# Kernel tuning notes

Hardware: AMD Instinct MI355X
Metric: run time of the kernel (lower is better)

Reference implementation:

```python
import jax, jax.numpy as jnp
import numpy as np

B, T, H, V, GEN = 1024, 64, 512, 1024, 100


def setup_inputs() -> dict:
    key = jax.random.key(0)
    ks = jax.random.split(key, 16)
    u = lambda k, shape, fan: jax.random.uniform(k, shape, jnp.float32, -1.0 / np.sqrt(fan), 1.0 / np.sqrt(fan))
    inp = {}
    inp["input"] = jax.random.normal(ks[0], (B, 1), jnp.float32)
    tok = jax.random.randint(ks[1], (B, T), 0, V)
    inp["onehots"] = jax.nn.one_hot(tok, V, dtype=jnp.float32)
    inp["digits"] = jax.random.randint(ks[2], (B,), 0, 10)
    inp["teacher"] = 0
    # expander_h / expander_c : Linear(1, H)
    inp["Wh"] = u(ks[3], (H, 1), 1); inp["bh"] = u(ks[4], (H,), 1)
    inp["Wc"] = u(ks[5], (H, 1), 1); inp["bc"] = u(ks[6], (H,), 1)
    # LSTM(V -> H), torch init: U(-1/sqrt(H), 1/sqrt(H)), gate order i,f,g,o
    inp["W_ih"] = u(ks[7], (4 * H, V), H); inp["W_hh"] = u(ks[8], (4 * H, H), H)
    inp["b_ih"] = u(ks[9], (4 * H,), H); inp["b_hh"] = u(ks[10], (4 * H,), H)
    # hidden2word: Linear(H, GEN) -> ReLU -> Linear(GEN, V) -> LogSoftmax
    inp["W1"] = u(ks[11], (GEN, H), H); inp["b1"] = u(ks[12], (GEN,), H)
    inp["W2"] = u(ks[13], (V, GEN), GEN); inp["b2"] = u(ks[14], (V,), GEN)
    return inp


def reference(input, onehots, digits, teacher, Wh, bh, Wc, bc, W_ih, W_hh, b_ih, b_hh, W1, b1, W2, b2):
    h0 = input @ Wh.T + bh  # [B,H]
    c0 = input @ Wc.T + bc  # [B,H]
    b = b_ih + b_hh

    def cell(h, c, x):
        g = x @ W_ih.T + h @ W_hh.T + b  # [B,4H]
        i, f, gg, o = jnp.split(g, 4, axis=-1)
        c = jax.nn.sigmoid(f) * c + jax.nn.sigmoid(i) * jnp.tanh(gg)
        h = jax.nn.sigmoid(o) * jnp.tanh(c)
        return h, c

    def head(h):  # hidden2word, log-softmax over vocab
        return jax.nn.log_softmax(jax.nn.relu(h @ W1.T + b1) @ W2.T + b2, axis=-1)

    if teacher:
        def step(carry, x):
            h, c = carry
            h, c = cell(h, c, x)
            return (h, c), head(h)
        _, logps = jax.lax.scan(step, (h0, c0), jnp.swapaxes(onehots, 0, 1))
    else:
        def step(carry, _):
            h, c, x = carry
            h, c = cell(h, c, x)
            logp = head(h)  # [B,V]
            nxt = jax.nn.one_hot(jnp.argmax(logp, axis=-1), V, dtype=logp.dtype)
            return (h, c, nxt), logp
        _, logps = jax.lax.scan(step, (h0, c0, onehots[:, 0, :]), None, length=T)
    return logps  # [T, B, V] == stacked vocab_list
```

## Files before the change

### kernel.cpp

```cpp
#include <hip/hip_runtime.h>
#include <math.h>

#define B_   1024
#define T_   64
#define H_   512
#define V_   1024
#define GEN_ 100
#define FH   2048
#define KC   1536

static constexpr size_t MB = 1024ull * 1024;
static constexpr size_t OFF_G    = 0;
static constexpr size_t OFF_C    = 16 * MB;
static constexpr size_t OFF_WIHT = 18 * MB;
static constexpr size_t OFF_ACAT = 26 * MB;
static constexpr size_t OFF_BCAT = 29 * MB;
static constexpr size_t OFF_BSUM = 35 * MB;
static constexpr size_t OFF_TOK  = 35 * MB + 8192;
static constexpr size_t OFF_H    = 36 * MB;

typedef __attribute__((ext_vector_type(8))) short short8v;
typedef __attribute__((ext_vector_type(4))) float f32x4;

__device__ __forceinline__ float sigf(float x) { return 1.0f / (1.0f + expf(-x)); }

__device__ __forceinline__ unsigned short f2bf(float f) {
    unsigned int u = __float_as_uint(f);
    return (unsigned short)((u + 0x7FFFu + ((u >> 16) & 1u)) >> 16);
}
__device__ __forceinline__ float bf2f(unsigned short b) {
    return __uint_as_float(((unsigned int)b) << 16);
}

__device__ __forceinline__ void gload16(const void* g, void* l) {
    __builtin_amdgcn_global_load_lds((const __attribute__((address_space(1))) void*)g,
                                     (__attribute__((address_space(3))) void*)l, 16, 0, 0);
}

__global__ __launch_bounds__(256) void k_init(const float* __restrict__ input,
                                              const float* __restrict__ Wh, const float* __restrict__ bh,
                                              const float* __restrict__ Wc, const float* __restrict__ bc,
                                              const float* __restrict__ bih, const float* __restrict__ bhh,
                                              float* __restrict__ cbuf, short* __restrict__ acat,
                                              float* __restrict__ bsum) {
    int idx = blockIdx.x * 256 + threadIdx.x;
    int b = idx >> 9, j = idx & (H_ - 1);
    float x = input[b];
    float h0 = x * Wh[j] + bh[j];
    cbuf[idx] = x * Wc[j] + bc[j];
    unsigned short hi = f2bf(h0);
    unsigned short lo = f2bf(h0 - bf2f(hi));
    short* ar = acat + (size_t)b * KC;
    ar[j] = (short)hi; ar[512 + j] = (short)hi; ar[1024 + j] = (short)lo;
    if (idx < FH) bsum[idx] = bih[idx] + bhh[idx];
}

__global__ __launch_bounds__(256) void k_tok0(const float* __restrict__ onehots, int* __restrict__ tok) {
    int idx = blockIdx.x * 256 + threadIdx.x;
    int b = idx >> 10, v = idx & (V_ - 1);
    if (onehots[(size_t)b * (T_ * V_) + v] > 0.5f) tok[b] = v;
}

__global__ __launch_bounds__(256) void k_transpose(const float* __restrict__ Wih, float* __restrict__ WihT) {
    int idx = blockIdx.x * 256 + threadIdx.x;
    int v = idx >> 11, n = idx & (FH - 1);
    WihT[idx] = Wih[(size_t)n * V_ + v];
}

__global__ __launch_bounds__(256) void k_prep(const float* __restrict__ Whh, short* __restrict__ bcat) {
    int idx = blockIdx.x * 256 + threadIdx.x;
    int n = idx >> 9, k = idx & (H_ - 1);
    float w = Whh[idx];
    unsigned short hi = f2bf(w);
    unsigned short lo = f2bf(w - bf2f(hi));
    short* br = bcat + (size_t)n * KC;
    br[k] = (short)hi; br[512 + k] = (short)lo; br[1024 + k] = (short)hi;
}

__global__ __launch_bounds__(256) void k_cell(const float* __restrict__ gbuf,
                                              float* __restrict__ cbuf, short* __restrict__ acat,
                                              const float* __restrict__ WihT, const float* __restrict__ bsum,
                                              const int* __restrict__ tok,
                                              float* __restrict__ hbuf) {
    const int tid = threadIdx.x;
    const int b = blockIdx.x * 2 + (tid >> 7);
    const int j = (tid & 127) << 2;
    const int tk = tok[b];
    const float* __restrict__ wr = WihT + (size_t)tk * FH;
    const size_t base = (size_t)b * FH;

    float4 g4[4];
#pragma unroll
    for (int gi_ = 0; gi_ < 4; ++gi_) {
        const int off = gi_ * 512 + j;
        float4 a0 = *(const float4*)&gbuf[base + off];
        float4 wv = *(const float4*)&wr[off];
        float4 bs = *(const float4*)&bsum[off];
        g4[gi_].x = a0.x + wv.x + bs.x;
        g4[gi_].y = a0.y + wv.y + bs.y;
        g4[gi_].z = a0.z + wv.z + bs.z;
        g4[gi_].w = a0.w + wv.w + bs.w;
    }
    float4 co = *(const float4*)&cbuf[(size_t)b * H_ + j];
    float cn[4], hn[4];
    const float* gi_p = (const float*)&g4[0];
    const float* gf_p = (const float*)&g4[1];
    const float* gg_p = (const float*)&g4[2];
    const float* go_p = (const float*)&g4[3];
    const float* co_p = (const float*)&co;
#pragma unroll
    for (int e = 0; e < 4; ++e) {
        cn[e] = sigf(gf_p[e]) * co_p[e] + sigf(gi_p[e]) * tanhf(gg_p[e]);
        hn[e] = sigf(go_p[e]) * tanhf(cn[e]);
    }
    *(float4*)&cbuf[(size_t)b * H_ + j] = make_float4(cn[0], cn[1], cn[2], cn[3]);
    *(float4*)&hbuf[(size_t)b * H_ + j] = make_float4(hn[0], hn[1], hn[2], hn[3]);
    unsigned long long hh = 0ull, ll = 0ull;
#pragma unroll
    for (int e = 0; e < 4; ++e) {
        unsigned short hi = f2bf(hn[e]);
        unsigned short lo = f2bf(hn[e] - bf2f(hi));
        hh |= (unsigned long long)hi << (16 * e);
        ll |= (unsigned long long)lo << (16 * e);
    }
    short* ar = acat + (size_t)b * KC;
    *(unsigned long long*)&ar[j]        = hh;
    *(unsigned long long*)&ar[512 + j]  = hh;
    *(unsigned long long*)&ar[1024 + j] = ll;
}

__global__ __launch_bounds__(256) void k_fused(int ngates,
                                               const short* __restrict__ Acat,
                                               const short* __restrict__ Bcat,
                                               float* __restrict__ gbuf,
                                               const float* __restrict__ hbuf,
                                               int* __restrict__ tok,
                                               const float* __restrict__ W1, const float* __restrict__ b1,
                                               const float* __restrict__ W2, const float* __restrict__ b2,
                                               float* __restrict__ outt) {
    const int tid = threadIdx.x;
    const int bj = blockIdx.x;

    union SMem {
        struct { short As[2][128 * 64]; short Bs[2][128 * 64]; } g;
        struct { float hs[4][512]; float pps[2][4][104]; float ps[4][104];
                 float red[4][4]; int redi[4][4]; } h;
    };
    __shared__ __align__(16) SMem sm;

    if (bj < ngates) {
        const int lane = tid & 63, w = tid >> 6;
        const int n0 = (bj & 15) * 128;
        const int m0 = (bj >> 4) * 128;

        f32x4 acc[4][4];
#pragma unroll
        for (int i = 0; i < 4; i++)
#pragma unroll
            for (int j = 0; j < 4; j++) acc[i][j] = (f32x4){0.f, 0.f, 0.f, 0.f};

        const int quad = lane >> 4, l15 = lane & 15;
        const int wm = (w >> 1) * 64, wn = (w & 1) * 64;

        const int srow = lane >> 3;
        const int schunk = (lane & 7) ^ srow;
        const size_t lanoff = (size_t)srow * KC + (size_t)schunk * 8;

        const short* aw = Acat + (size_t)(m0 + w * 32) * KC + lanoff;
        const short* bw = Bcat + (size_t)(n0 + w * 32) * KC + lanoff;

        int raA[4], rxA[4], raB[4], rxB[4];
#pragma unroll
        for (int i = 0; i < 4; i++) {
            int rm = wm + i * 16 + l15; raA[i] = rm * 8; rxA[i] = rm & 7;
            int rn = wn + i * 16 + l15; raB[i] = rn * 8; rxB[i] = rn & 7;
        }

#pragma unroll
        for (int u = 0; u < 4; ++u) {
            gload16(aw + (size_t)(u * 8) * KC, &sm.g.As[0][w * 2048] + u * 512);
            gload16(bw + (size_t)(u * 8) * KC, &sm.g.Bs[0][w * 2048] + u * 512);
        }
        __syncthreads();
#pragma unroll 2
        for (int it = 0; it < 24; ++it) {
            if (it < 23) {
                const int nb = (it + 1) & 1;
                const short* ga = aw + (it + 1) * 64;
                const short* gb = bw + (it + 1) * 64;
#pragma unroll
                for (int u = 0; u < 4; ++u) {
                    gload16(ga + (size_t)(u * 8) * KC, &sm.g.As[nb][w * 2048] + u * 512);
                    gload16(gb + (size_t)(u * 8) * KC, &sm.g.Bs[nb][w * 2048] + u * 512);
                }
            }
            const short* Ab = &sm.g.As[it & 1][0];
            const short* Bb = &sm.g.Bs[it & 1][0];
#pragma unroll
            for (int kh = 0; kh < 2; ++kh) {
                const int c = kh * 4 + quad;
                short8v av[4], bv[4];
#pragma unroll
                for (int i = 0; i < 4; i++) av[i] = *(const short8v*)&Ab[(raA[i] + (c ^ rxA[i])) * 8];
#pragma unroll
                for (int j = 0; j < 4; j++) bv[j] = *(const short8v*)&Bb[(raB[j] + (c ^ rxB[j])) * 8];
#pragma unroll
                for (int i = 0; i < 4; i++)
#pragma unroll
                    for (int j = 0; j < 4; j++)
                        acc[i][j] = __builtin_amdgcn_mfma_f32_16x16x32_bf16(av[i], bv[j], acc[i][j], 0, 0, 0);
            }
            __syncthreads();
        }

#pragma unroll
        for (int i = 0; i < 4; i++) {
            const int m = m0 + wm + i * 16 + quad * 4;
#pragma unroll
            for (int j = 0; j < 4; j++) {
                const int n = n0 + wn + j * 16 + l15;
                float* gp = gbuf + (size_t)m * FH + n;
#pragma unroll
                for (int r = 0; r < 4; r++) gp[(size_t)r * FH] = acc[i][j][r];
            }
        }
        return;
    }

    const int b0 = (bj - ngates) * 4;

    for (int idx = tid; idx < 512; idx += 256) {
        const int r = idx >> 7, jq = (idx & 127) << 2;
        *(float4*)&sm.h.hs[r][jq] = *(const float4*)&hbuf[(size_t)(b0 + r) * H_ + jq];
    }
    __syncthreads();

    if (tid < 200) {
        const int gi2 = tid % 100, kq = tid / 100;
        const float4* __restrict__ wrow = (const float4*)(W1 + (size_t)gi2 * H_ + kq * 256);
        float a0 = 0.f, a1 = 0.f, a2 = 0.f, a3 = 0.f;
#pragma unroll 4
        for (int k4 = 0; k4 < 64; k4++) {
            float4 w  = wrow[k4];
            float4 h0 = *(const float4*)&sm.h.hs[0][kq * 256 + k4 * 4];
            float4 h1 = *(const float4*)&sm.h.hs[1][kq * 256 + k4 * 4];
            float4 h2 = *(const float4*)&sm.h.hs[2][kq * 256 + k4 * 4];
            float4 h3 = *(const float4*)&sm.h.hs[3][kq * 256 + k4 * 4];
            a0 += w.x * h0.x + w.y * h0.y + w.z * h0.z + w.w * h0.w;
            a1 += w.x * h1.x + w.y * h1.y + w.z * h1.z + w.w * h1.w;
            a2 += w.x * h2.x + w.y * h2.y + w.z * h2.z + w.w * h2.w;
            a3 += w.x * h3.x + w.y * h3.y + w.z * h3.z + w.w * h3.w;
        }
        sm.h.pps[kq][0][gi2] = a0; sm.h.pps[kq][1][gi2] = a1;
        sm.h.pps[kq][2][gi2] = a2; sm.h.pps[kq][3][gi2] = a3;
    }
    __syncthreads();
    for (int idx = tid; idx < 400; idx += 256) {
        const int r = idx / 100, gi2 = idx % 100;
        float v = b1[gi2] + sm.h.pps[0][r][gi2] + sm.h.pps[1][r][gi2];
        sm.h.ps[r][gi2] = v > 0.f ? v : 0.f;
    }
    __syncthreads();

    const int v0 = tid * 4;
    float accv[4][4];
#pragma unroll
    for (int vi = 0; vi < 4; vi++) {
        const float bb = b2[v0 + vi];
#pragma unroll
        for (int r = 0; r < 4; r++) accv[vi][r] = bb;
    }
#pragma unroll 5
    for (int j4 = 0; j4 < 25; j4++) {
        float4 p0 = *(const float4*)&sm.h.ps[0][j4 * 4];
        float4 p1 = *(const float4*)&sm.h.ps[1][j4 * 4];
        float4 p2 = *(const float4*)&sm.h.ps[2][j4 * 4];
        float4 p3 = *(const float4*)&sm.h.ps[3][j4 * 4];
#pragma unroll
        for (int vi = 0; vi < 4; vi++) {
            float4 w = *(const float4*)&W2[(size_t)(v0 + vi) * GEN_ + j4 * 4];
            accv[vi][0] += w.x * p0.x + w.y * p0.y + w.z * p0.z + w.w * p0.w;
            accv[vi][1] += w.x * p1.x + w.y * p1.y + w.z * p1.z + w.w * p1.w;
            accv[vi][2] += w.x * p2.x + w.y * p2.y + w.z * p2.z + w.w * p2.w;
            accv[vi][3] += w.x * p3.x + w.y * p3.y + w.z * p3.z + w.w * p3.w;
        }
    }

    float lmax[4]; int lidx[4];
#pragma unroll
    for (int r = 0; r < 4; r++) {
        lmax[r] = accv[0][r]; lidx[r] = v0;
#pragma unroll
        for (int vi = 1; vi < 4; vi++)
            if (accv[vi][r] > lmax[r]) { lmax[r] = accv[vi][r]; lidx[r] = v0 + vi; }
    }
#pragma unroll
    for (int off = 32; off; off >>= 1) {
#pragma unroll
        for (int r = 0; r < 4; r++) {
            float ov = __shfl_xor(lmax[r], off);
            int   oi = __shfl_xor(lidx[r], off);
            if (ov > lmax[r] || (ov == lmax[r] && oi < lidx[r])) { lmax[r] = ov; lidx[r] = oi; }
        }
    }
    const int wv = tid >> 6, lane = tid & 63;
    if (lane == 0) {
#pragma unroll
        for (int r = 0; r < 4; r++) { sm.h.red[r][wv] = lmax[r]; sm.h.redi[r][wv] = lidx[r]; }
    }
    __syncthreads();
    float rmax[4]; int ridx[4];
#pragma unroll
    for (int r = 0; r < 4; r++) {
        rmax[r] = sm.h.red[r][0]; ridx[r] = sm.h.redi[r][0];
#pragma unroll
        for (int w = 1; w < 4; w++)
            if (sm.h.red[r][w] > rmax[r] || (sm.h.red[r][w] == rmax[r] && sm.h.redi[r][w] < ridx[r])) {
                rmax[r] = sm.h.red[r][w]; ridx[r] = sm.h.redi[r][w];
            }
    }
    __syncthreads();

    float ls[4];
#pragma unroll
    for (int r = 0; r < 4; r++)
        ls[r] = expf(accv[0][r] - rmax[r]) + expf(accv[1][r] - rmax[r]) +
                expf(accv[2][r] - rmax[r]) + expf(accv[3][r] - rmax[r]);
#pragma unroll
    for (int off = 32; off; off >>= 1) {
#pragma unroll
        for (int r = 0; r < 4; r++) ls[r] += __shfl_xor(ls[r], off);
    }
    if (lane == 0) {
#pragma unroll
        for (int r = 0; r < 4; r++) sm.h.red[r][wv] = ls[r];
    }
    __syncthreads();
#pragma unroll
    for (int r = 0; r < 4; r++) {
        const float logZ = rmax[r] + logf(sm.h.red[r][0] + sm.h.red[r][1] + sm.h.red[r][2] + sm.h.red[r][3]);
        float4 o;
        o.x = accv[0][r] - logZ; o.y = accv[1][r] - logZ;
        o.z = accv[2][r] - logZ; o.w = accv[3][r] - logZ;
        *(float4*)&outt[(size_t)(b0 + r) * V_ + v0] = o;
    }
    if (tid == 0) {
        tok[b0 + 0] = ridx[0]; tok[b0 + 1] = ridx[1];
        tok[b0 + 2] = ridx[2]; tok[b0 + 3] = ridx[3];
    }
}

extern "C" void kernel_launch(void* const* d_in, const int* in_sizes, int n_in,
                              void* d_out, int out_size, void* d_ws, size_t ws_size,
                              hipStream_t stream) {
    const float* input   = (const float*)d_in[0];
    const float* onehots = (const float*)d_in[1];
    const float* Wh  = (const float*)d_in[4];
    const float* bh  = (const float*)d_in[5];
    const float* Wc  = (const float*)d_in[6];
    const float* bc  = (const float*)d_in[7];
    const float* Wih = (const float*)d_in[8];
    const float* Whh = (const float*)d_in[9];
    const float* bih = (const float*)d_in[10];
    const float* bhh = (const float*)d_in[11];
    const float* W1  = (const float*)d_in[12];
    const float* b1  = (const float*)d_in[13];
    const float* W2  = (const float*)d_in[14];
    const float* b2  = (const float*)d_in[15];
    float* out = (float*)d_out;

    char* ws = (char*)d_ws;
    float* gbuf  = (float*)(ws + OFF_G);
    float* cbuf  = (float*)(ws + OFF_C);
    float* WihT  = (float*)(ws + OFF_WIHT);
    short* acat  = (short*)(ws + OFF_ACAT);
    short* bcat  = (short*)(ws + OFF_BCAT);
    float* bsum  = (float*)(ws + OFF_BSUM);
    int*   tok   = (int*)(ws + OFF_TOK);
    float* hbuf  = (float*)(ws + OFF_H);

    k_init<<<(B_ * H_) / 256, 256, 0, stream>>>(input, Wh, bh, Wc, bc, bih, bhh, cbuf, acat, bsum);
    k_tok0<<<(B_ * V_) / 256, 256, 0, stream>>>(onehots, tok);
    k_transpose<<<(V_ * FH) / 256, 256, 0, stream>>>(Wih, WihT);
    k_prep<<<(FH * H_) / 256, 256, 0, stream>>>(Whh, bcat);

    k_fused<<<128, 256, 0, stream>>>(128, acat, bcat, gbuf, hbuf, tok,
                                     W1, b1, W2, b2, out);

    for (int t = 0; t < T_; t++) {
        k_cell<<<B_ / 2, 256, 0, stream>>>(gbuf, cbuf, acat, WihT, bsum, tok, hbuf);
        const int ngates = (t < T_ - 1) ? 128 : 0;
        k_fused<<<ngates + 256, 256, 0, stream>>>(ngates, acat, bcat, gbuf, hbuf, tok,
                                                  W1, b1, W2, b2, out + (size_t)t * B_ * V_);
    }
}
```

Measured before the change: 3.793 ms.

## Use 512-thread blocks in fused GEMM/head kernel and fold bias into WihT

Doubles the block size of the fused kernel to 8 waves, each handling a 64x32 sub-tile of the gate GEMM and 2 vocab entries in the head, so that each block has more waves to hide latency and less register work per thread. The reductions are widened to 8 waves. Separately, the summed LSTM bias is folded into the transposed input weights once during setup, removing one load per gate in the per-step cell kernel. The risk is more synchronisation cost per block and lower occupancy per compute unit with 512-thread blocks.

```diff
diff --git a/kernel.cpp b/kernel.cpp
--- a/kernel.cpp
+++ b/kernel.cpp
@@ -61,10 +61,12 @@
     if (onehots[(size_t)b * (T_ * V_) + v] > 0.5f) tok[b] = v;
 }
 
-__global__ __launch_bounds__(256) void k_transpose(const float* __restrict__ Wih, float* __restrict__ WihT) {
+__global__ __launch_bounds__(256) void k_transpose(const float* __restrict__ Wih,
+                                                   const float* __restrict__ bsum,
+                                                   float* __restrict__ WihT) {
     int idx = blockIdx.x * 256 + threadIdx.x;
     int v = idx >> 11, n = idx & (FH - 1);
-    WihT[idx] = Wih[(size_t)n * V_ + v];
+    WihT[idx] = Wih[(size_t)n * V_ + v] + bsum[n];
 }
 
 __global__ __launch_bounds__(256) void k_prep(const float* __restrict__ Whh, short* __restrict__ bcat) {
@@ -79,7 +81,7 @@
 
 __global__ __launch_bounds__(256) void k_cell(const float* __restrict__ gbuf,
                                               float* __restrict__ cbuf, short* __restrict__ acat,
-                                              const float* __restrict__ WihT, const float* __restrict__ bsum,
+                                              const float* __restrict__ WihT,
                                               const int* __restrict__ tok,
                                               float* __restrict__ hbuf) {
     const int tid = threadIdx.x;
@@ -95,11 +97,10 @@
         const int off = gi_ * 512 + j;
         float4 a0 = *(const float4*)&gbuf[base + off];
         float4 wv = *(const float4*)&wr[off];
-        float4 bs = *(const float4*)&bsum[off];
-        g4[gi_].x = a0.x + wv.x + bs.x;
-        g4[gi_].y = a0.y + wv.y + bs.y;
-        g4[gi_].z = a0.z + wv.z + bs.z;
-        g4[gi_].w = a0.w + wv.w + bs.w;
+        g4[gi_].x = a0.x + wv.x;
+        g4[gi_].y = a0.y + wv.y;
+        g4[gi_].z = a0.z + wv.z;
+        g4[gi_].w = a0.w + wv.w;
     }
     float4 co = *(const float4*)&cbuf[(size_t)b * H_ + j];
     float cn[4], hn[4];
@@ -129,7 +130,7 @@
     *(unsigned long long*)&ar[1024 + j] = ll;
 }
 
-__global__ __launch_bounds__(256) void k_fused(int ngates,
+__global__ __launch_bounds__(512) void k_fused(int ngates,
                                                const short* __restrict__ Acat,
                                                const short* __restrict__ Bcat,
                                                float* __restrict__ gbuf,
@@ -144,42 +145,43 @@
     union SMem {
         struct { short As[2][128 * 64]; short Bs[2][128 * 64]; } g;
         struct { float hs[4][512]; float pps[2][4][104]; float ps[4][104];
-                 float red[4][4]; int redi[4][4]; } h;
+                 float red[4][8]; int redi[4][8]; } h;
     };
     __shared__ __align__(16) SMem sm;
 
+    const int lane = tid & 63, wv = tid >> 6;
+    const int quad = lane >> 4, l15 = lane & 15;
+
     if (bj < ngates) {
-        const int lane = tid & 63, w = tid >> 6;
         const int n0 = (bj & 15) * 128;
         const int m0 = (bj >> 4) * 128;
-
-        f32x4 acc[4][4];
-#pragma unroll
-        for (int i = 0; i < 4; i++)
-#pragma unroll
-            for (int j = 0; j < 4; j++) acc[i][j] = (f32x4){0.f, 0.f, 0.f, 0.f};
-
-        const int quad = lane >> 4, l15 = lane & 15;
-        const int wm = (w >> 1) * 64, wn = (w & 1) * 64;
+        const int wm = (wv >> 2) * 64;
+        const int wn = (wv & 3) * 32;
+
+        f32x4 acc[4][2];
+#pragma unroll
+        for (int i = 0; i < 4; i++) {
+            acc[i][0] = (f32x4){0.f, 0.f, 0.f, 0.f};
+            acc[i][1] = (f32x4){0.f, 0.f, 0.f, 0.f};
+        }
 
         const int srow = lane >> 3;
         const int schunk = (lane & 7) ^ srow;
         const size_t lanoff = (size_t)srow * KC + (size_t)schunk * 8;
 
-        const short* aw = Acat + (size_t)(m0 + w * 32) * KC + lanoff;
-        const short* bw = Bcat + (size_t)(n0 + w * 32) * KC + lanoff;
-
-        int raA[4], rxA[4], raB[4], rxB[4];
-#pragma unroll
-        for (int i = 0; i < 4; i++) {
-            int rm = wm + i * 16 + l15; raA[i] = rm * 8; rxA[i] = rm & 7;
-            int rn = wn + i * 16 + l15; raB[i] = rn * 8; rxB[i] = rn & 7;
-        }
-
-#pragma unroll
-        for (int u = 0; u < 4; ++u) {
-            gload16(aw + (size_t)(u * 8) * KC, &sm.g.As[0][w * 2048] + u * 512);
-            gload16(bw + (size_t)(u * 8) * KC, &sm.g.Bs[0][w * 2048] + u * 512);
+        const short* aw = Acat + (size_t)(m0 + wv * 16) * KC + lanoff;
+        const short* bw = Bcat + (size_t)(n0 + wv * 16) * KC + lanoff;
+
+        int raA[4], rxA[4], raB[2], rxB[2];
+#pragma unroll
+        for (int i = 0; i < 4; i++) { int rm = wm + i * 16 + l15; raA[i] = rm * 8; rxA[i] = rm & 7; }
+#pragma unroll
+        for (int j = 0; j < 2; j++) { int rn = wn + j * 16 + l15; raB[j] = rn * 8; rxB[j] = rn & 7; }
+
+#pragma unroll
+        for (int u = 0; u < 2; ++u) {
+            gload16(aw + (size_t)(u * 8) * KC, &sm.g.As[0][wv * 1024] + u * 512);
+            gload16(bw + (size_t)(u * 8) * KC, &sm.g.Bs[0][wv * 1024] + u * 512);
         }
         __syncthreads();
 #pragma unroll 2
@@ -189,9 +191,9 @@
                 const short* ga = aw + (it + 1) * 64;
                 const short* gb = bw + (it + 1) * 64;
 #pragma unroll
-                for (int u = 0; u < 4; ++u) {
-                    gload16(ga + (size_t)(u * 8) * KC, &sm.g.As[nb][w * 2048] + u * 512);
-                    gload16(gb + (size_t)(u * 8) * KC, &sm.g.Bs[nb][w * 2048] + u * 512);
+                for (int u = 0; u < 2; ++u) {
+                    gload16(ga + (size_t)(u * 8) * KC, &sm.g.As[nb][wv * 1024] + u * 512);
+                    gload16(gb + (size_t)(u * 8) * KC, &sm.g.Bs[nb][wv * 1024] + u * 512);
                 }
             }
             const short* Ab = &sm.g.As[it & 1][0];
@@ -199,16 +201,16 @@
 #pragma unroll
             for (int kh = 0; kh < 2; ++kh) {
                 const int c = kh * 4 + quad;
-                short8v av[4], bv[4];
+                short8v av[4], bv[2];
 #pragma unroll
                 for (int i = 0; i < 4; i++) av[i] = *(const short8v*)&Ab[(raA[i] + (c ^ rxA[i])) * 8];
 #pragma unroll
-                for (int j = 0; j < 4; j++) bv[j] = *(const short8v*)&Bb[(raB[j] + (c ^ rxB[j])) * 8];
-#pragma unroll
-                for (int i = 0; i < 4; i++)
-#pragma unroll
-                    for (int j = 0; j < 4; j++)
-                        acc[i][j] = __builtin_amdgcn_mfma_f32_16x16x32_bf16(av[i], bv[j], acc[i][j], 0, 0, 0);
+                for (int j = 0; j < 2; j++) bv[j] = *(const short8v*)&Bb[(raB[j] + (c ^ rxB[j])) * 8];
+#pragma unroll
+                for (int i = 0; i < 4; i++) {
+                    acc[i][0] = __builtin_amdgcn_mfma_f32_16x16x32_bf16(av[i], bv[0], acc[i][0], 0, 0, 0);
+                    acc[i][1] = __builtin_amdgcn_mfma_f32_16x16x32_bf16(av[i], bv[1], acc[i][1], 0, 0, 0);
+                }
             }
             __syncthreads();
         }
@@ -217,7 +219,7 @@
         for (int i = 0; i < 4; i++) {
             const int m = m0 + wm + i * 16 + quad * 4;
 #pragma unroll
-            for (int j = 0; j < 4; j++) {
+            for (int j = 0; j < 2; j++) {
                 const int n = n0 + wn + j * 16 + l15;
                 float* gp = gbuf + (size_t)m * FH + n;
 #pragma unroll
@@ -229,8 +231,8 @@
 
     const int b0 = (bj - ngates) * 4;
 
-    for (int idx = tid; idx < 512; idx += 256) {
-        const int r = idx >> 7, jq = (idx & 127) << 2;
+    {
+        const int r = tid >> 7, jq = (tid & 127) << 2;
         *(float4*)&sm.h.hs[r][jq] = *(const float4*)&hbuf[(size_t)(b0 + r) * H_ + jq];
     }
     __syncthreads();
@@ -255,17 +257,17 @@
         sm.h.pps[kq][2][gi2] = a2; sm.h.pps[kq][3][gi2] = a3;
     }
     __syncthreads();
-    for (int idx = tid; idx < 400; idx += 256) {
-        const int r = idx / 100, gi2 = idx % 100;
+    if (tid < 400) {
+        const int r = tid / 100, gi2 = tid % 100;
         float v = b1[gi2] + sm.h.pps[0][r][gi2] + sm.h.pps[1][r][gi2];
         sm.h.ps[r][gi2] = v > 0.f ? v : 0.f;
     }
     __syncthreads();
 
-    const int v0 = tid * 4;
-    float accv[4][4];
-#pragma unroll
-    for (int vi = 0; vi < 4; vi++) {
+    const int v0 = tid * 2;
+    float accv[2][4];
+#pragma unroll
+    for (int vi = 0; vi < 2; vi++) {
         const float bb = b2[v0 + vi];
 #pragma unroll
         for (int r = 0; r < 4; r++) accv[vi][r] = bb;
@@ -277,7 +279,7 @@
         float4 p2 = *(const float4*)&sm.h.ps[2][j4 * 4];
         float4 p3 = *(const float4*)&sm.h.ps[3][j4 * 4];
 #pragma unroll
-        for (int vi = 0; vi < 4; vi++) {
+        for (int vi = 0; vi < 2; vi++) {
             float4 w = *(const float4*)&W2[(size_t)(v0 + vi) * GEN_ + j4 * 4];
             accv[vi][0] += w.x * p0.x + w.y * p0.y + w.z * p0.z + w.w * p0.w;
             accv[vi][1] += w.x * p1.x + w.y * p1.y + w.z * p1.z + w.w * p1.w;
@@ -290,9 +292,7 @@
 #pragma unroll
     for (int r = 0; r < 4; r++) {
         lmax[r] = accv[0][r]; lidx[r] = v0;
-#pragma unroll
-        for (int vi = 1; vi < 4; vi++)
-            if (accv[vi][r] > lmax[r]) { lmax[r] = accv[vi][r]; lidx[r] = v0 + vi; }
+        if (accv[1][r] > lmax[r]) { lmax[r] = accv[1][r]; lidx[r] = v0 + 1; }
     }
 #pragma unroll
     for (int off = 32; off; off >>= 1) {
@@ -303,7 +303,6 @@
             if (ov > lmax[r] || (ov == lmax[r] && oi < lidx[r])) { lmax[r] = ov; lidx[r] = oi; }
         }
     }
-    const int wv = tid >> 6, lane = tid & 63;
     if (lane == 0) {
 #pragma unroll
         for (int r = 0; r < 4; r++) { sm.h.red[r][wv] = lmax[r]; sm.h.redi[r][wv] = lidx[r]; }
@@ -314,9 +313,9 @@
     for (int r = 0; r < 4; r++) {
         rmax[r] = sm.h.red[r][0]; ridx[r] = sm.h.redi[r][0];
 #pragma unroll
-        for (int w = 1; w < 4; w++)
-            if (sm.h.red[r][w] > rmax[r] || (sm.h.red[r][w] == rmax[r] && sm.h.redi[r][w] < ridx[r])) {
-                rmax[r] = sm.h.red[r][w]; ridx[r] = sm.h.redi[r][w];
+        for (int w2 = 1; w2 < 8; w2++)
+            if (sm.h.red[r][w2] > rmax[r] || (sm.h.red[r][w2] == rmax[r] && sm.h.redi[r][w2] < ridx[r])) {
+                rmax[r] = sm.h.red[r][w2]; ridx[r] = sm.h.redi[r][w2];
             }
     }
     __syncthreads();
@@ -324,8 +323,7 @@
     float ls[4];
 #pragma unroll
     for (int r = 0; r < 4; r++)
-        ls[r] = expf(accv[0][r] - rmax[r]) + expf(accv[1][r] - rmax[r]) +
-                expf(accv[2][r] - rmax[r]) + expf(accv[3][r] - rmax[r]);
+        ls[r] = expf(accv[0][r] - rmax[r]) + expf(accv[1][r] - rmax[r]);
 #pragma unroll
     for (int off = 32; off; off >>= 1) {
 #pragma unroll
@@ -338,15 +336,17 @@
     __syncthreads();
 #pragma unroll
     for (int r = 0; r < 4; r++) {
-        const float logZ = rmax[r] + logf(sm.h.red[r][0] + sm.h.red[r][1] + sm.h.red[r][2] + sm.h.red[r][3]);
-        float4 o;
+        float tot = sm.h.red[r][0];
+#pragma unroll
+        for (int w2 = 1; w2 < 8; w2++) tot += sm.h.red[r][w2];
+        const float logZ = rmax[r] + logf(tot);
+        float2 o;
         o.x = accv[0][r] - logZ; o.y = accv[1][r] - logZ;
-        o.z = accv[2][r] - logZ; o.w = accv[3][r] - logZ;
-        *(float4*)&outt[(size_t)(b0 + r) * V_ + v0] = o;
+        *(float2*)&outt[(size_t)(b0 + r) * V_ + v0] = o;
     }
     if (tid == 0) {
-        tok[b0 + 0] = ridx[0]; tok[b0 + 1] = ridx[1];
-        tok[b0 + 2] = ridx[2]; tok[b0 + 3] = ridx[3];
+#pragma unroll
+        for (int r = 0; r < 4; r++) tok[b0 + r] = ridx[r];
     }
 }
 
@@ -381,16 +381,16 @@
 
     k_init<<<(B_ * H_) / 256, 256, 0, stream>>>(input, Wh, bh, Wc, bc, bih, bhh, cbuf, acat, bsum);
     k_tok0<<<(B_ * V_) / 256, 256, 0, stream>>>(onehots, tok);
-    k_transpose<<<(V_ * FH) / 256, 256, 0, stream>>>(Wih, WihT);
+    k_transpose<<<(V_ * FH) / 256, 256, 0, stream>>>(Wih, bsum, WihT);
     k_prep<<<(FH * H_) / 256, 256, 0, stream>>>(Whh, bcat);
 
-    k_fused<<<128, 256, 0, stream>>>(128, acat, bcat, gbuf, hbuf, tok,
+    k_fused<<<128, 512, 0, stream>>>(128, acat, bcat, gbuf, hbuf, tok,
                                      W1, b1, W2, b2, out);
 
     for (int t = 0; t < T_; t++) {
-        k_cell<<<B_ / 2, 256, 0, stream>>>(gbuf, cbuf, acat, WihT, bsum, tok, hbuf);
+        k_cell<<<B_ / 2, 256, 0, stream>>>(gbuf, cbuf, acat, WihT, tok, hbuf);
         const int ngates = (t < T_ - 1) ? 128 : 0;
-        k_fused<<<ngates + 256, 256, 0, stream>>>(ngates, acat, bcat, gbuf, hbuf, tok,
+        k_fused<<<ngates + 256, 512, 0, stream>>>(ngates, acat, bcat, gbuf, hbuf, tok,
                                                   W1, b1, W2, b2, out + (size_t)t * B_ * V_);
     }
 }
```

New measurement: 3.813 ms. No clear change (+0.5%).
